# Optimization experiments

Measured on AMD Instinct MI355X. Metric: run time of the kernel, lower is better.

The kernel has to match this reference:

```python
import jax, jax.numpy as jnp
import numpy as np

DIM = 256
NUM_HEADS = 8
AGENT_NUM = 49
POOL = 7  # int(sqrt(agent_num))


def setup_inputs() -> dict:
    key = jax.random.key(0)
    k1, k2, k3, k4, k5 = jax.random.split(key, 5)
    x = jax.random.normal(k1, (8, 8, 8, 14, 14, DIM), dtype=jnp.float32)
    wq = jax.random.normal(k2, (DIM, DIM), dtype=jnp.float32) * 0.02
    wkv = jax.random.normal(k3, (2 * DIM, DIM), dtype=jnp.float32) * 0.02
    w_proj = jax.random.normal(k4, (DIM, DIM), dtype=jnp.float32) * 0.02
    b_proj = jax.random.normal(k5, (DIM,), dtype=jnp.float32) * 0.02
    return {"x": x, "wq": wq, "wkv": wkv, "w_proj": w_proj, "b_proj": b_proj}


def reference(x, wq, wkv, w_proj, b_proj):
    B, Hh, Ww, wh, ww, c = x.shape
    b = B * Hh * Ww
    n = wh * ww
    H, W = ww, wh  # module uses (H, W) = (window_width, window_height)
    nh = NUM_HEADS
    hd = c // nh
    scale = hd ** -0.5

    xt = x.reshape(b, n, c)  # (b x y)(w1 w2) d
    q = xt @ wq.T                          # [b, n, c]
    kv = xt @ wkv.T                        # [b, n, 2c]
    k, v = kv[..., :c], kv[..., c:]

    # agent tokens: adaptive avg pool q over the window grid to POOL x POOL
    qs = q.reshape(b, H, W, c)
    agent = qs.reshape(b, POOL, H // POOL, POOL, W // POOL, c).mean(axis=(2, 4))
    agent = agent.reshape(b, AGENT_NUM, c)

    # split heads -> [b, nh, seq, hd]
    qh = q.reshape(b, n, nh, hd).transpose(0, 2, 1, 3)
    kh = k.reshape(b, n, nh, hd).transpose(0, 2, 1, 3)
    vh = v.reshape(b, n, nh, hd).transpose(0, 2, 1, 3)
    ah = agent.reshape(b, AGENT_NUM, nh, hd).transpose(0, 2, 1, 3)

    # stage 1: agents attend over k/v
    agent_attn = jax.nn.softmax(jnp.einsum('bhad,bhnd->bhan', ah * scale, kh), axis=-1)
    agent_v = jnp.einsum('bhan,bhnd->bhad', agent_attn, vh)

    # stage 2: queries attend over agents
    q_attn = jax.nn.softmax(jnp.einsum('bhnd,bhad->bhna', qh * scale, ah), axis=-1)
    out = jnp.einsum('bhna,bhad->bhnd', q_attn, agent_v)

    out = out.transpose(0, 2, 1, 3).reshape(b, n, c)
    out = out @ w_proj.T + b_proj
    # rearrange '(b x y) (i j) c -> b x y i j c' with i = window_width
    return out.reshape(B, Hh, Ww, ww, wh, c)
```

## Files before the change

### kernel.cpp

```cpp
#include <hip/hip_runtime.h>

typedef unsigned short u16;
typedef __attribute__((ext_vector_type(8))) short bf16x8;
typedef __attribute__((ext_vector_type(4))) float f32x4;

#define M_ROWS 100352
#define NB     512
#define NTOK   196
#define CDIM   256
#define NHEADS 8
#define HDIM   32
#define ANUM   49

__device__ __forceinline__ u16 f2bf(float f) {
    union { float f; unsigned u; } c; c.f = f;
    return (u16)((c.u + 0x7FFFu + ((c.u >> 16) & 1u)) >> 16);
}
__device__ __forceinline__ float bf2f(u16 u) {
    union { unsigned u; float f; } c; c.u = ((unsigned)u) << 16;
    return c.f;
}

#define NX4 6422528
__global__ __launch_bounds__(256)
void cast_all(const float* __restrict__ x, const float* __restrict__ wq,
              const float* __restrict__ wkv, const float* __restrict__ wproj,
              u16* __restrict__ xb, u16* __restrict__ wqkvb,
              u16* __restrict__ wprojb)
{
    const int idx4 = blockIdx.x * 256 + threadIdx.x;
    const float* src; u16* dst; int off;
    if (idx4 < NX4)               { src = x;     dst = xb;             off = idx4; }
    else if (idx4 < NX4 + 16384)  { src = wq;    dst = wqkvb;          off = idx4 - NX4; }
    else if (idx4 < NX4 + 49152)  { src = wkv;   dst = wqkvb + 65536;  off = idx4 - NX4 - 16384; }
    else                          { src = wproj; dst = wprojb;         off = idx4 - NX4 - 49152; }
    float4 v = *reinterpret_cast<const float4*>(&src[(size_t)off * 4]);
    ushort4 o;
    o.x = f2bf(v.x); o.y = f2bf(v.y); o.z = f2bf(v.z); o.w = f2bf(v.w);
    *reinterpret_cast<ushort4*>(&dst[(size_t)off * 4]) = o;
}

#define GLD 40
__global__ __launch_bounds__(256)
void gemm_qkv(const u16* __restrict__ xb, const u16* __restrict__ wqkvb,
              u16* __restrict__ qb, u16* __restrict__ kvb)
{
    __shared__ u16 As[128 * GLD];
    __shared__ u16 Bs[128 * GLD];

    const int tid  = threadIdx.x;
    const int lane = tid & 63, wid = tid >> 6;
    const int wm = wid >> 1, wn = wid & 1;
    const int row0 = blockIdx.x * 128;
    const int col0 = blockIdx.y * 128;

    f32x4 acc[4][4] = {};
    const int lrow = lane & 15;
    const int lk   = (lane >> 4) * 8;

    for (int k0 = 0; k0 < 256; k0 += 32) {
        #pragma unroll
        for (int i = 0; i < 2; ++i) {
            const int c = tid + i * 256;
            const int r = c >> 2, kc = c & 3;
            bf16x8 va = *reinterpret_cast<const bf16x8*>(
                &xb[(size_t)(row0 + r) * 256 + k0 + kc * 8]);
            *reinterpret_cast<bf16x8*>(&As[r * GLD + kc * 8]) = va;
            bf16x8 vb = *reinterpret_cast<const bf16x8*>(
                &wqkvb[(size_t)(col0 + r) * 256 + k0 + kc * 8]);
            *reinterpret_cast<bf16x8*>(&Bs[r * GLD + kc * 8]) = vb;
        }
        __syncthreads();

        bf16x8 af[4], bfr[4];
        #pragma unroll
        for (int m = 0; m < 4; ++m)
            af[m] = *reinterpret_cast<bf16x8*>(&As[(wm*64 + m*16 + lrow) * GLD + lk]);
        #pragma unroll
        for (int n = 0; n < 4; ++n)
            bfr[n] = *reinterpret_cast<bf16x8*>(&Bs[(wn*64 + n*16 + lrow) * GLD + lk]);
        #pragma unroll
        for (int m = 0; m < 4; ++m)
            #pragma unroll
            for (int n = 0; n < 4; ++n)
                acc[m][n] = __builtin_amdgcn_mfma_f32_16x16x32_bf16(
                                af[m], bfr[n], acc[m][n], 0, 0, 0);
        __syncthreads();
    }

    const bool isq = (col0 < 256);
    u16* C = isq ? qb : kvb;
    const int ldc = isq ? 256 : 512;
    const int cb  = isq ? col0 : col0 - 256;
    #pragma unroll
    for (int n = 0; n < 4; ++n) {
        const int ccol = cb + wn*64 + n*16 + (lane & 15);
        #pragma unroll
        for (int m = 0; m < 4; ++m) {
            const int rbase = row0 + wm*64 + m*16 + (lane >> 4) * 4;
            #pragma unroll
            for (int r = 0; r < 4; ++r)
                C[(size_t)(rbase + r) * ldc + ccol] = f2bf(acc[m][n][r]);
        }
    }
}

__global__ __launch_bounds__(256)
void gemm_proj(const u16* __restrict__ A, const u16* __restrict__ Bw,
               const float* __restrict__ bias, float* __restrict__ C)
{
    __shared__ u16 As[128 * GLD];
    __shared__ u16 Bs[128 * GLD];

    const int tid  = threadIdx.x;
    const int lane = tid & 63, wid = tid >> 6;
    const int wm = wid >> 1, wn = wid & 1;
    const int row0 = blockIdx.x * 128;
    const int col0 = blockIdx.y * 128;

    f32x4 acc[4][4] = {};
    const int lrow = lane & 15;
    const int lk   = (lane >> 4) * 8;

    for (int k0 = 0; k0 < 256; k0 += 32) {
        #pragma unroll
        for (int i = 0; i < 2; ++i) {
            const int c = tid + i * 256;
            const int r = c >> 2, kc = c & 3;
            bf16x8 va = *reinterpret_cast<const bf16x8*>(
                &A[(size_t)(row0 + r) * 256 + k0 + kc * 8]);
            *reinterpret_cast<bf16x8*>(&As[r * GLD + kc * 8]) = va;
            bf16x8 vb = *reinterpret_cast<const bf16x8*>(
                &Bw[(size_t)(col0 + r) * 256 + k0 + kc * 8]);
            *reinterpret_cast<bf16x8*>(&Bs[r * GLD + kc * 8]) = vb;
        }
        __syncthreads();

        bf16x8 af[4], bfr[4];
        #pragma unroll
        for (int m = 0; m < 4; ++m)
            af[m] = *reinterpret_cast<bf16x8*>(&As[(wm*64 + m*16 + lrow) * GLD + lk]);
        #pragma unroll
        for (int n = 0; n < 4; ++n)
            bfr[n] = *reinterpret_cast<bf16x8*>(&Bs[(wn*64 + n*16 + lrow) * GLD + lk]);
        #pragma unroll
        for (int m = 0; m < 4; ++m)
            #pragma unroll
            for (int n = 0; n < 4; ++n)
                acc[m][n] = __builtin_amdgcn_mfma_f32_16x16x32_bf16(
                                af[m], bfr[n], acc[m][n], 0, 0, 0);
        __syncthreads();
    }

    #pragma unroll
    for (int n = 0; n < 4; ++n) {
        const int ccol = col0 + wn*64 + n*16 + (lane & 15);
        const float bv = bias[ccol];
        #pragma unroll
        for (int m = 0; m < 4; ++m) {
            const int rbase = row0 + wm*64 + m*16 + (lane >> 4) * 4;
            #pragma unroll
            for (int r = 0; r < 4; ++r)
                C[(size_t)(rbase + r) * 256 + ccol] = acc[m][n][r] + bv;
        }
    }
}

#define SA_LD   40
#define SVT_LD  232
#define SP1_LD  232
#define SAVT_LD 72
#define SP2_LD  72
#define OFF_A   0
#define OFF_VT  2560
#define OFF_P1  9984
#define OFF_AVT 24832
#define OFF_P2  2560
#define LDS_U16 27136

__global__ __launch_bounds__(256, 3)
void fused_attn(const u16* __restrict__ kvb, u16* __restrict__ qb)
{
    __shared__ __align__(16) u16 lds[LDS_U16];
    const int tid  = threadIdx.x;
    const int lane = tid & 63, w = tid >> 6;
    const int li = lane & 15, g = lane >> 4;
    const int b = blockIdx.x >> 3, h = blockIdx.x & 7;
    const float scale = 0.1767766952966369f;
    const f32x4 z = {0.f, 0.f, 0.f, 0.f};
    const bf16x8 zv = {0,0,0,0,0,0,0,0};
    const ushort4 z4 = {0,0,0,0};

    for (int i = tid; i < 60; i += 256) {
        const int row = 49 + (i >> 2), kc = i & 3;
        *reinterpret_cast<bf16x8*>(&lds[OFF_A + row * SA_LD + kc * 8]) = zv;
    }
    for (int i = tid; i < 224; i += 256) {
        const int row = i / 7, c4 = 196 + (i % 7) * 4;
        *reinterpret_cast<ushort4*>(&lds[OFF_VT + row * SVT_LD + c4]) = z4;
    }
    for (int i = tid; i < 128; i += 256) {
        const int row = i >> 1, c = 208 + (i & 1) * 8;
        *reinterpret_cast<bf16x8*>(&lds[OFF_P1 + row * SP1_LD + c]) = zv;
    }

    const u16* qslice = qb + (size_t)b * NTOK * CDIM + h * HDIM;
    for (int i = tid; i < ANUM * 8; i += 256) {
        const int a = i >> 3, dq = (i & 7) * 4;
        const int p1 = a / 7, p2 = a - p1 * 7;
        float s0 = 0.f, s1 = 0.f, s2 = 0.f, s3 = 0.f;
        #pragma unroll
        for (int i2 = 0; i2 < 2; ++i2)
            #pragma unroll
            for (int j2 = 0; j2 < 2; ++j2) {
                const int n = (p1*2 + i2) * 14 + p2*2 + j2;
                ushort4 v = *reinterpret_cast<const ushort4*>(
                    &qslice[(size_t)n * CDIM + dq]);
                s0 += bf2f(v.x); s1 += bf2f(v.y);
                s2 += bf2f(v.z); s3 += bf2f(v.w);
            }
        const float cc = 0.25f * scale;
        ushort4 o;
        o.x = f2bf(s0 * cc); o.y = f2bf(s1 * cc);
        o.z = f2bf(s2 * cc); o.w = f2bf(s3 * cc);
        *reinterpret_cast<ushort4*>(&lds[OFF_A + a * SA_LD + dq]) = o;
    }

    for (int i = tid; i < NTOK * 2; i += 256) {
        const int n = i >> 1, dh = i & 1;
        const u16* src = &kvb[((size_t)(b * NTOK + n)) * 512 + 256 + h * HDIM + dh * 16];
        bf16x8 v0 = *reinterpret_cast<const bf16x8*>(src);
        bf16x8 v1 = *reinterpret_cast<const bf16x8*>(src + 8);
        #pragma unroll
        for (int j2 = 0; j2 < 8; ++j2) {
            lds[OFF_VT + (dh * 16 + j2) * SVT_LD + n]     = (u16)v0[j2];
            lds[OFF_VT + (dh * 16 + 8 + j2) * SVT_LD + n] = (u16)v1[j2];
        }
    }
    __syncthreads();

    {
        bf16x8 af = *reinterpret_cast<bf16x8*>(&lds[OFF_A + (w*16 + li) * SA_LD + g*8]);
        f32x4 c[13];
        #pragma unroll
        for (int j = 0; j < 13; ++j) {
            int krow = j*16 + li; krow = krow > 195 ? 195 : krow;
            bf16x8 kf = *reinterpret_cast<const bf16x8*>(
                &kvb[((size_t)(b * NTOK + krow)) * 512 + h * HDIM + g*8]);
            c[j] = __builtin_amdgcn_mfma_f32_16x16x32_bf16(af, kf, z, 0, 0, 0);
        }
        #pragma unroll
        for (int r = 0; r < 4; ++r) {
            float m = -1e30f;
            #pragma unroll
            for (int j = 0; j < 13; ++j)
                if (j < 12 || li < 4) m = fmaxf(m, c[j][r]);
            #pragma unroll
            for (int d = 1; d < 16; d <<= 1) m = fmaxf(m, __shfl_xor(m, d));
            float p[13]; float su = 0.f;
            #pragma unroll
            for (int j = 0; j < 13; ++j) {
                p[j] = (j < 12 || li < 4) ? __expf(c[j][r] - m) : 0.f;
                su += p[j];
            }
            #pragma unroll
            for (int d = 1; d < 16; d <<= 1) su += __shfl_xor(su, d);
            const float inv = 1.f / su;
            const int arow = w*16 + g*4 + r;
            #pragma unroll
            for (int j = 0; j < 13; ++j)
                lds[OFF_P1 + arow * SP1_LD + j*16 + li] = f2bf(p[j] * inv);
        }
    }
    __syncthreads();

    #pragma unroll
    for (int dt = 0; dt < 2; ++dt) {
        f32x4 acc = z;
        #pragma unroll
        for (int kk = 0; kk < 7; ++kk) {
            bf16x8 pa = *reinterpret_cast<bf16x8*>(
                &lds[OFF_P1 + (w*16 + li) * SP1_LD + kk*32 + g*8]);
            bf16x8 vb = *reinterpret_cast<bf16x8*>(
                &lds[OFF_VT + (dt*16 + li) * SVT_LD + kk*32 + g*8]);
            acc = __builtin_amdgcn_mfma_f32_16x16x32_bf16(pa, vb, acc, 0, 0, 0);
        }
        #pragma unroll
        for (int r = 0; r < 4; ++r)
            lds[OFF_AVT + (dt*16 + li) * SAVT_LD + w*16 + g*4 + r] = f2bf(acc[r]);
    }
    __syncthreads();

    {
        bf16x8 ab[4];
        #pragma unroll
        for (int at = 0; at < 4; ++at)
            ab[at] = *reinterpret_cast<bf16x8*>(&lds[OFF_A + (at*16 + li) * SA_LD + g*8]);
        for (int j = w; j < 13; j += 4) {
            const int qrow = min(j*16 + li, NTOK - 1);
            bf16x8 qf = *reinterpret_cast<const bf16x8*>(
                &qb[((size_t)(b * NTOK) + qrow) * CDIM + h * HDIM + g*8]);
            f32x4 cc[4];
            #pragma unroll
            for (int at = 0; at < 4; ++at)
                cc[at] = __builtin_amdgcn_mfma_f32_16x16x32_bf16(qf, ab[at], z, 0, 0, 0);
            #pragma unroll
            for (int r = 0; r < 4; ++r) {
                float m = -1e30f;
                #pragma unroll
                for (int at = 0; at < 4; ++at)
                    if (at < 3 || li < 1) m = fmaxf(m, cc[at][r]);
                #pragma unroll
                for (int d = 1; d < 16; d <<= 1) m = fmaxf(m, __shfl_xor(m, d));
                float p[4]; float su = 0.f;
                #pragma unroll
                for (int at = 0; at < 4; ++at) {
                    p[at] = (at < 3 || li < 1) ? __expf(cc[at][r] - m) : 0.f;
                    su += p[at];
                }
                #pragma unroll
                for (int d = 1; d < 16; d <<= 1) su += __shfl_xor(su, d);
                const float inv = 1.f / su;
                const int trow = j*16 + g*4 + r;
                #pragma unroll
                for (int at = 0; at < 4; ++at)
                    lds[OFF_P2 + trow * SP2_LD + at*16 + li] = f2bf(p[at] * inv);
            }
        }
    }
    __syncthreads();

    for (int j = w; j < 13; j += 4) {
        #pragma unroll
        for (int dt = 0; dt < 2; ++dt) {
            f32x4 acc = z;
            #pragma unroll
            for (int kk = 0; kk < 2; ++kk) {
                bf16x8 pf = *reinterpret_cast<bf16x8*>(
                    &lds[OFF_P2 + (j*16 + li) * SP2_LD + kk*32 + g*8]);
                bf16x8 avf = *reinterpret_cast<bf16x8*>(
                    &lds[OFF_AVT + (dt*16 + li) * SAVT_LD + kk*32 + g*8]);
                acc = __builtin_amdgcn_mfma_f32_16x16x32_bf16(pf, avf, acc, 0, 0, 0);
            }
            #pragma unroll
            for (int r = 0; r < 4; ++r) {
                const int t = j*16 + g*4 + r;
                if (t < NTOK)
                    qb[((size_t)(b * NTOK) + t) * CDIM + h * HDIM + dt*16 + li]
                        = f2bf(acc[r]);
            }
        }
    }
}

extern "C" void kernel_launch(void* const* d_in, const int* in_sizes, int n_in,
                              void* d_out, int out_size, void* d_ws, size_t ws_size,
                              hipStream_t stream)
{
    const float* x     = (const float*)d_in[0];
    const float* wq    = (const float*)d_in[1];
    const float* wkv   = (const float*)d_in[2];
    const float* wproj = (const float*)d_in[3];
    const float* bproj = (const float*)d_in[4];
    float* out = (float*)d_out;

    u16* wqkvb  = (u16*)d_ws;
    u16* wprojb = wqkvb  + 196608;
    u16* xb     = wprojb + 65536;
    u16* qb     = xb     + (size_t)M_ROWS * CDIM;
    u16* kvb    = qb     + (size_t)M_ROWS * CDIM;

    const dim3 blk(256);

    cast_all<<<dim3(25344), blk, 0, stream>>>(x, wq, wkv, wproj, xb, wqkvb, wprojb);
    gemm_qkv<<<dim3(M_ROWS/128, 6), blk, 0, stream>>>(xb, wqkvb, qb, kvb);
    fused_attn<<<dim3(NB*NHEADS), blk, 0, stream>>>(kvb, qb);
    gemm_proj<<<dim3(M_ROWS/128, 2), blk, 0, stream>>>(qb, wprojb, bproj, out);
}
```

Baseline: 448.5 us.

## Store Q/K/V in head-major planar layout for contiguous attention access

The QKV GEMM epilogue now scatters outputs into separate Q, K, V buffers laid out as [batch*head][token][32], so each attention block reads one contiguous 12.5KB slice instead of 64-byte strided pieces. The attention kernel and the projection GEMM's A-loads are rewritten to use this layout, with the projection gathering per-head chunks. The aim is better coalescing and cache-line use in the attention kernel. The cost is a per-row divide by 196 in both GEMMs, and GEMM epilogue stores that each cover only 32-element runs.

```diff
diff --git a/kernel.cpp b/kernel.cpp
--- a/kernel.cpp
+++ b/kernel.cpp
@@ -11,6 +11,7 @@
 #define NHEADS 8
 #define HDIM   32
 #define ANUM   49
+#define PLSTRIDE 6272
 
 __device__ __forceinline__ u16 f2bf(float f) {
     union { float f; unsigned u; } c; c.f = f;
@@ -43,7 +44,7 @@
 #define GLD 40
 __global__ __launch_bounds__(256)
 void gemm_qkv(const u16* __restrict__ xb, const u16* __restrict__ wqkvb,
-              u16* __restrict__ qb, u16* __restrict__ kvb)
+              u16* __restrict__ qh, u16* __restrict__ kh, u16* __restrict__ vh)
 {
     __shared__ u16 As[128 * GLD];
     __shared__ u16 Bs[128 * GLD];
@@ -88,25 +89,29 @@
         __syncthreads();
     }
 
-    const bool isq = (col0 < 256);
-    u16* C = isq ? qb : kvb;
-    const int ldc = isq ? 256 : 512;
-    const int cb  = isq ? col0 : col0 - 256;
     #pragma unroll
     for (int n = 0; n < 4; ++n) {
-        const int ccol = cb + wn*64 + n*16 + (lane & 15);
+        const int ccol = col0 + wn*64 + n*16 + (lane & 15);
+        const int pl = ccol >> 8;
+        const int hh = (ccol >> 5) & 7;
+        const int d  = ccol & 31;
+        u16* base = (pl == 0) ? qh : (pl == 1) ? kh : vh;
         #pragma unroll
         for (int m = 0; m < 4; ++m) {
             const int rbase = row0 + wm*64 + m*16 + (lane >> 4) * 4;
             #pragma unroll
-            for (int r = 0; r < 4; ++r)
-                C[(size_t)(rbase + r) * ldc + ccol] = f2bf(acc[m][n][r]);
+            for (int r = 0; r < 4; ++r) {
+                const unsigned row = rbase + r;
+                const unsigned bb = row / 196u;
+                const unsigned nn = row - bb * 196u;
+                base[((size_t)(bb*8 + hh) * 196 + nn) * 32 + d] = f2bf(acc[m][n][r]);
+            }
         }
     }
 }
 
 __global__ __launch_bounds__(256)
-void gemm_proj(const u16* __restrict__ A, const u16* __restrict__ Bw,
+void gemm_proj(const u16* __restrict__ qh, const u16* __restrict__ Bw,
                const float* __restrict__ bias, float* __restrict__ C)
 {
     __shared__ u16 As[128 * GLD];
@@ -123,12 +128,16 @@
     const int lk   = (lane >> 4) * 8;
 
     for (int k0 = 0; k0 < 256; k0 += 32) {
+        const int hh = k0 >> 5;
         #pragma unroll
         for (int i = 0; i < 2; ++i) {
             const int c = tid + i * 256;
             const int r = c >> 2, kc = c & 3;
+            const unsigned row = row0 + r;
+            const unsigned bb = row / 196u;
+            const unsigned nn = row - bb * 196u;
             bf16x8 va = *reinterpret_cast<const bf16x8*>(
-                &A[(size_t)(row0 + r) * 256 + k0 + kc * 8]);
+                &qh[((size_t)(bb*8 + hh) * 196 + nn) * 32 + kc * 8]);
             *reinterpret_cast<bf16x8*>(&As[r * GLD + kc * 8]) = va;
             bf16x8 vb = *reinterpret_cast<const bf16x8*>(
                 &Bw[(size_t)(col0 + r) * 256 + k0 + kc * 8]);
@@ -179,18 +188,23 @@
 #define LDS_U16 27136
 
 __global__ __launch_bounds__(256, 3)
-void fused_attn(const u16* __restrict__ kvb, u16* __restrict__ qb)
+void fused_attn(const u16* __restrict__ kh, const u16* __restrict__ vh,
+                u16* __restrict__ qh)
 {
     __shared__ __align__(16) u16 lds[LDS_U16];
     const int tid  = threadIdx.x;
     const int lane = tid & 63, w = tid >> 6;
     const int li = lane & 15, g = lane >> 4;
-    const int b = blockIdx.x >> 3, h = blockIdx.x & 7;
+    const int bh = blockIdx.x;
     const float scale = 0.1767766952966369f;
     const f32x4 z = {0.f, 0.f, 0.f, 0.f};
     const bf16x8 zv = {0,0,0,0,0,0,0,0};
     const ushort4 z4 = {0,0,0,0};
 
+    const u16* ksl = kh + (size_t)bh * PLSTRIDE;
+    const u16* vsl = vh + (size_t)bh * PLSTRIDE;
+    u16*       qsl = qh + (size_t)bh * PLSTRIDE;
+
     for (int i = tid; i < 60; i += 256) {
         const int row = 49 + (i >> 2), kc = i & 3;
         *reinterpret_cast<bf16x8*>(&lds[OFF_A + row * SA_LD + kc * 8]) = zv;
@@ -204,7 +218,6 @@
         *reinterpret_cast<bf16x8*>(&lds[OFF_P1 + row * SP1_LD + c]) = zv;
     }
 
-    const u16* qslice = qb + (size_t)b * NTOK * CDIM + h * HDIM;
     for (int i = tid; i < ANUM * 8; i += 256) {
         const int a = i >> 3, dq = (i & 7) * 4;
         const int p1 = a / 7, p2 = a - p1 * 7;
@@ -214,8 +227,7 @@
             #pragma unroll
             for (int j2 = 0; j2 < 2; ++j2) {
                 const int n = (p1*2 + i2) * 14 + p2*2 + j2;
-                ushort4 v = *reinterpret_cast<const ushort4*>(
-                    &qslice[(size_t)n * CDIM + dq]);
+                ushort4 v = *reinterpret_cast<const ushort4*>(&qsl[n * 32 + dq]);
                 s0 += bf2f(v.x); s1 += bf2f(v.y);
                 s2 += bf2f(v.z); s3 += bf2f(v.w);
             }
@@ -226,16 +238,12 @@
         *reinterpret_cast<ushort4*>(&lds[OFF_A + a * SA_LD + dq]) = o;
     }
 
-    for (int i = tid; i < NTOK * 2; i += 256) {
-        const int n = i >> 1, dh = i & 1;
-        const u16* src = &kvb[((size_t)(b * NTOK + n)) * 512 + 256 + h * HDIM + dh * 16];
-        bf16x8 v0 = *reinterpret_cast<const bf16x8*>(src);
-        bf16x8 v1 = *reinterpret_cast<const bf16x8*>(src + 8);
-        #pragma unroll
-        for (int j2 = 0; j2 < 8; ++j2) {
-            lds[OFF_VT + (dh * 16 + j2) * SVT_LD + n]     = (u16)v0[j2];
-            lds[OFF_VT + (dh * 16 + 8 + j2) * SVT_LD + n] = (u16)v1[j2];
-        }
+    for (int i = tid; i < NTOK * 4; i += 256) {
+        const int n = i >> 2, dc = i & 3;
+        bf16x8 v = *reinterpret_cast<const bf16x8*>(&vsl[i * 8]);
+        #pragma unroll
+        for (int j2 = 0; j2 < 8; ++j2)
+            lds[OFF_VT + (dc * 8 + j2) * SVT_LD + n] = (u16)v[j2];
     }
     __syncthreads();
 
@@ -245,8 +253,7 @@
         #pragma unroll
         for (int j = 0; j < 13; ++j) {
             int krow = j*16 + li; krow = krow > 195 ? 195 : krow;
-            bf16x8 kf = *reinterpret_cast<const bf16x8*>(
-                &kvb[((size_t)(b * NTOK + krow)) * 512 + h * HDIM + g*8]);
+            bf16x8 kf = *reinterpret_cast<const bf16x8*>(&ksl[krow * 32 + g*8]);
             c[j] = __builtin_amdgcn_mfma_f32_16x16x32_bf16(af, kf, z, 0, 0, 0);
         }
         #pragma unroll
@@ -298,8 +305,7 @@
             ab[at] = *reinterpret_cast<bf16x8*>(&lds[OFF_A + (at*16 + li) * SA_LD + g*8]);
         for (int j = w; j < 13; j += 4) {
             const int qrow = min(j*16 + li, NTOK - 1);
-            bf16x8 qf = *reinterpret_cast<const bf16x8*>(
-                &qb[((size_t)(b * NTOK) + qrow) * CDIM + h * HDIM + g*8]);
+            bf16x8 qf = *reinterpret_cast<const bf16x8*>(&qsl[qrow * 32 + g*8]);
             f32x4 cc[4];
             #pragma unroll
             for (int at = 0; at < 4; ++at)
@@ -346,8 +352,7 @@
             for (int r = 0; r < 4; ++r) {
                 const int t = j*16 + g*4 + r;
                 if (t < NTOK)
-                    qb[((size_t)(b * NTOK) + t) * CDIM + h * HDIM + dt*16 + li]
-                        = f2bf(acc[r]);
+                    qsl[t * 32 + dt*16 + li] = f2bf(acc[r]);
             }
         }
     }
@@ -367,13 +372,14 @@
     u16* wqkvb  = (u16*)d_ws;
     u16* wprojb = wqkvb  + 196608;
     u16* xb     = wprojb + 65536;
-    u16* qb     = xb     + (size_t)M_ROWS * CDIM;
-    u16* kvb    = qb     + (size_t)M_ROWS * CDIM;
+    u16* qh     = xb     + (size_t)M_ROWS * CDIM;
+    u16* kh     = qh     + (size_t)M_ROWS * CDIM;
+    u16* vh     = kh     + (size_t)M_ROWS * CDIM;
 
     const dim3 blk(256);
 
     cast_all<<<dim3(25344), blk, 0, stream>>>(x, wq, wkv, wproj, xb, wqkvb, wprojb);
-    gemm_qkv<<<dim3(M_ROWS/128, 6), blk, 0, stream>>>(xb, wqkvb, qb, kvb);
-    fused_attn<<<dim3(NB*NHEADS), blk, 0, stream>>>(kvb, qb);
-    gemm_proj<<<dim3(M_ROWS/128, 2), blk, 0, stream>>>(qb, wprojb, bproj, out);
-}
+    gemm_qkv<<<dim3(M_ROWS/128, 6), blk, 0, stream>>>(xb, wqkvb, qh, kh, vh);
+    fused_attn<<<dim3(NB*NHEADS), blk, 0, stream>>>(kh, vh, qh);
+    gemm_proj<<<dim3(M_ROWS/128, 2), blk, 0, stream>>>(qh, wprojb, bproj, out);
+}
```

New measurement: 403.2 us. -10.1%, faster.
